# Performance work log

Measured on AMD Instinct MI355X. Metric: run time of the kernel, lower is better.

Reference implementation:

```python
import jax, jax.numpy as jnp
import numpy as np

N = 3        # n_agents (hard-coded by obs.reshape(3,-1) and range(42) loop)
H = 2048     # rnn_hidden_dim
A = 512      # attention_dim
F = 42       # input_shape - n_agents
TAU = 0.01   # gumbel softmax temperature
IDX = np.array([[j for j in range(N) if j != i] for i in range(N)])  # [N, N-1] neighbors in ascending order


def _gru_cell(x, h, Wih, Whh, bih, bhh):
    # PyTorch GRUCell math; weights stacked [r; z; n] along dim 0.
    gi = x @ Wih.T + bih
    gh = h @ Whh.T + bhh
    ir, iz, in_ = jnp.split(gi, 3, axis=-1)
    hr, hz, hn = jnp.split(gh, 3, axis=-1)
    r = jax.nn.sigmoid(ir + hr)
    z = jax.nn.sigmoid(iz + hz)
    n = jnp.tanh(in_ + r * hn)
    return (1.0 - z) * n + z * h


def setup_inputs() -> dict:
    ks = jax.random.split(jax.random.key(0), 24)
    s = 0.02
    rn = lambda k, shp: (jax.random.normal(k, shp) * s).astype(jnp.float32)
    return {
        "obs": jax.random.normal(ks[0], (N, F), dtype=jnp.float32),
        "hidden_state": jax.random.normal(ks[1], (N, H), dtype=jnp.float32),
        "gumbel_noise": jax.random.gumbel(ks[2], (N * (N - 1), 2), dtype=jnp.float32),
        "W_enc": rn(ks[3], (H, F)), "b_enc": rn(ks[4], (H,)),
        "Wih_c": rn(ks[5], (3 * H, H)), "Whh_c": rn(ks[6], (3 * H, H)),
        "bih_c": rn(ks[7], (3 * H,)), "bhh_c": rn(ks[8], (3 * H,)),
        "Wih_f": rn(ks[9], (3 * H, 2 * H)), "Whh_f": rn(ks[10], (3 * H, H)),
        "bih_f": rn(ks[11], (3 * H,)), "bhh_f": rn(ks[12], (3 * H,)),
        "Wih_r": rn(ks[13], (3 * H, 2 * H)), "Whh_r": rn(ks[14], (3 * H, H)),
        "bih_r": rn(ks[15], (3 * H,)), "bhh_r": rn(ks[16], (3 * H,)),
        "W_hard": rn(ks[17], (2, 2 * H)), "b_hard": rn(ks[18], (2,)),
        "Wq": rn(ks[19], (A, H)), "Wk": rn(ks[20], (A, H)),
    }


def reference(obs, hidden_state, gumbel_noise, W_enc, b_enc, Wih_c, Whh_c, bih_c, bhh_c,
              Wih_f, Whh_f, bih_f, bhh_f, Wih_r, Whh_r, bih_r, bhh_r,
              W_hard, b_hard, Wq, Wk):
    # encode + GRUCell step
    x = jax.nn.relu(obs @ W_enc.T + b_enc)                 # [3, H]
    h_out = _gru_cell(x, hidden_state, Wih_c, Whh_c, bih_c, bhh_c)  # [3, H]
    h = h_out.reshape(1, N, H)                              # B=1

    # pairwise concatenations (i, j!=i), seq-major for the bi-GRU
    nbr = h[:, IDX]                                         # [1, N, N-1, H]
    self_rep = jnp.broadcast_to(h[:, :, None, :], nbr.shape)
    pair = jnp.concatenate([self_rep, nbr], axis=-1)        # [1, N, N-1, 2H]
    seq = pair.transpose(2, 0, 1, 3).reshape(N - 1, N, 2 * H)  # [seq=N-1, batch=B*N, 2H]

    h0 = jnp.zeros((N, H), dtype=seq.dtype)

    def step_f(hc, xt):
        hn = _gru_cell(xt, hc, Wih_f, Whh_f, bih_f, bhh_f)
        return hn, hn

    def step_r(hc, xt):
        hn = _gru_cell(xt, hc, Wih_r, Whh_r, bih_r, bhh_r)
        return hn, hn

    _, outs_f = jax.lax.scan(step_f, h0, seq)
    _, outs_r = jax.lax.scan(step_r, h0, seq[::-1])
    h_hard = jnp.concatenate([outs_f, outs_r[::-1]], axis=-1)  # [N-1, N, 2H]
    h_hard = h_hard.transpose(1, 0, 2).reshape(-1, 2 * H)      # [N*(N-1), 2H]

    # hard gate: gumbel-softmax (soft, tau=0.01), take class-1 prob
    logits = h_hard @ W_hard.T + b_hard                      # [N*(N-1), 2]
    y = jax.nn.softmax((logits + gumbel_noise) / TAU, axis=-1)
    hw = y[:, 1].reshape(1, N, 1, N - 1).transpose(1, 0, 2, 3)  # [N, 1, 1, N-1]

    # per-agent masked attention over other agents
    q = (h_out @ Wq.T).reshape(1, N, A)
    k = (h_out @ Wk.T).reshape(1, N, A)
    k_nb = k[:, IDX]                                         # [1, N, N-1, A]
    scores = jnp.einsum('bia,bija->bij', q, k_nb) / jnp.sqrt(jnp.asarray(A, q.dtype))
    soft = jax.nn.softmax(scores, axis=-1)                   # [1, N, N-1]
    xx = soft[0] * hw[:, 0, 0, :]                            # [N, N-1]

    # pairwise squared-distance / duplicate-pair flag logic (vectorized)
    obs3 = obs.reshape(3, -1)                                # [3, 42]
    diff = obs3[:, None, :] - obs3[IDX]                      # [3, 2, 42]
    res = jnp.sum(diff * diff, axis=-1)                      # [3, 2]
    jloc = jnp.argmax(res, axis=1)
    maxv = jnp.take_along_axis(res, jloc[:, None], axis=1)[:, 0]
    iarr = jnp.arange(3)
    jadj = jnp.where((maxv != 0) & (jloc >= iarr), jloc + 1, jloc)
    lo = jnp.minimum(iarr, jadj)
    hi = jnp.maximum(iarr, jadj)
    temp = jnp.stack([lo, hi], axis=-1).astype(jnp.int32)    # [3, 2]
    eq01 = jnp.all(temp[0] == temp[1])
    eq02 = jnp.all(temp[0] == temp[2])
    eq12 = jnp.all(temp[1] == temp[2])
    none = jnp.array([-1, -1], dtype=jnp.int32)              # encodes original flag==0
    flag = jnp.where(eq12, temp[1], jnp.where(eq01 | eq02, temp[0], none))
    return h_out, xx, flag
```

## Files before the change

kernel.cpp:

```cpp
#include <hip/hip_runtime.h>
#include <math.h>

#define HU 2048
#define H3 6144

__device__ __forceinline__ float dot4(float4 a, float4 b){
  return a.x*b.x + a.y*b.y + a.z*b.z + a.w*b.w;
}
__device__ __forceinline__ float wred(float v){
  #pragma unroll
  for (int off = 32; off > 0; off >>= 1) v += __shfl_down(v, off, 64);
  return v;
}
__device__ __forceinline__ float sigm(float x){ return 1.0f/(1.0f + __expf(-x)); }

__global__ void k_enc(const float* __restrict__ obs, const float* __restrict__ W,
                      const float* __restrict__ b, float* __restrict__ x){
  __shared__ float so[128];
  int tid = threadIdx.x;
  if (tid < 126) so[tid] = obs[tid];
  __syncthreads();
  int r = blockIdx.x * blockDim.x + tid;
  if (r < HU){
    const float* wr = W + r*42;
    float a0=0.f, a1=0.f, a2=0.f;
    #pragma unroll
    for (int k2 = 0; k2 < 42; ++k2){
      float w = wr[k2];
      a0 += w*so[k2]; a1 += w*so[42+k2]; a2 += w*so[84+k2];
    }
    float bb = b[r];
    x[r]        = fmaxf(a0+bb, 0.f);
    x[HU + r]   = fmaxf(a1+bb, 0.f);
    x[2*HU + r] = fmaxf(a2+bb, 0.f);
  }
}

__global__ __launch_bounds__(256) void k_gemv2k(
    const float* __restrict__ W0, const float* __restrict__ X0,
    const float* __restrict__ b0, float* __restrict__ O0,
    const float* __restrict__ W1, const float* __restrict__ X1,
    const float* __restrict__ b1, float* __restrict__ O1){
  int blk = blockIdx.x;
  int seg = (blk >= 768);
  const float* W    = seg ? W1 : W0;
  const float* X    = seg ? X1 : X0;
  const float* bias = seg ? b1 : b0;
  float* O          = seg ? O1 : O0;
  int tid = threadIdx.x;
  int wave = tid >> 6, lane = tid & 63;
  int r0 = (((seg ? blk - 768 : blk) * 4 + wave) * 2);
  const float4* W4 = (const float4*)W;
  const float4* X4 = (const float4*)X;
  float acc[2][3];
  acc[0][0]=0.f; acc[0][1]=0.f; acc[0][2]=0.f;
  acc[1][0]=0.f; acc[1][1]=0.f; acc[1][2]=0.f;
  #pragma unroll 2
  for (int win = 0; win < 8; ++win){
    int xi = win*64 + lane;
    float4 x0 = X4[xi], x1 = X4[512 + xi], x2 = X4[1024 + xi];
    float4 w0 = W4[(size_t)r0*512 + xi];
    float4 w1 = W4[(size_t)r0*512 + 512 + xi];
    acc[0][0] += dot4(w0,x0); acc[0][1] += dot4(w0,x1); acc[0][2] += dot4(w0,x2);
    acc[1][0] += dot4(w1,x0); acc[1][1] += dot4(w1,x1); acc[1][2] += dot4(w1,x2);
  }
  #pragma unroll
  for (int j = 0; j < 2; ++j){
    float a0 = wred(acc[j][0]), a1 = wred(acc[j][1]), a2 = wred(acc[j][2]);
    if (lane == 0){
      int row = r0 + j;
      float bb = bias[row];
      O[row] = a0 + bb; O[H3 + row] = a1 + bb; O[2*H3 + row] = a2 + bb;
    }
  }
}

__global__ void k_gate_c(const float* __restrict__ gi, const float* __restrict__ gh,
                         const float* __restrict__ hprev,
                         float* __restrict__ hout_ws, float* __restrict__ dout){
  int id = blockIdx.x * blockDim.x + threadIdx.x;
  if (id >= 3*HU) return;
  int b = id >> 11, u = id & 2047;
  const float* gib = gi + b*H3;
  const float* ghb = gh + b*H3;
  float r = sigm(gib[u]      + ghb[u]);
  float z = sigm(gib[HU+u]   + ghb[HU+u]);
  float n = tanhf(gib[2*HU+u] + r*ghb[2*HU+u]);
  float h = hprev[id];
  float o = (1.f - z)*n + z*h;
  hout_ws[id] = o;
  dout[id] = o;
}

__global__ __launch_bounds__(256) void k_ih(
    const float* __restrict__ Wf, const float* __restrict__ bf, float* __restrict__ giF,
    const float* __restrict__ Wr_, const float* __restrict__ br, float* __restrict__ giR,
    const float* __restrict__ Wq, float* __restrict__ q,
    const float* __restrict__ Wk, float* __restrict__ kk,
    const float* __restrict__ hout){
  int blk = blockIdx.x;
  int tid = threadIdx.x;
  int wave = tid >> 6, lane = tid & 63;
  const float4* X4 = (const float4*)hout;
  if (blk < 1536){
    int segr = (blk >= 768);
    const float* W    = segr ? Wr_ : Wf;
    const float* bias = segr ? br  : bf;
    float* gi         = segr ? giR : giF;
    int r0 = (((segr ? blk - 768 : blk) * 4 + wave) * 2);
    const float4* W4 = (const float4*)W;
    float accS[2][3], accN[2][3];
    accS[0][0]=0.f; accS[0][1]=0.f; accS[0][2]=0.f;
    accS[1][0]=0.f; accS[1][1]=0.f; accS[1][2]=0.f;
    accN[0][0]=0.f; accN[0][1]=0.f; accN[0][2]=0.f;
    accN[1][0]=0.f; accN[1][1]=0.f; accN[1][2]=0.f;
    #pragma unroll 2
    for (int win = 0; win < 8; ++win){
      int xi = win*64 + lane;
      float4 x0 = X4[xi], x1 = X4[512 + xi], x2 = X4[1024 + xi];
      float4 w0 = W4[(size_t)r0*1024 + xi];
      float4 w1 = W4[(size_t)r0*1024 + 1024 + xi];
      accS[0][0] += dot4(w0,x0); accS[0][1] += dot4(w0,x1); accS[0][2] += dot4(w0,x2);
      accS[1][0] += dot4(w1,x0); accS[1][1] += dot4(w1,x1); accS[1][2] += dot4(w1,x2);
    }
    #pragma unroll 2
    for (int win = 0; win < 8; ++win){
      int xi = win*64 + lane;
      float4 x0 = X4[xi], x1 = X4[512 + xi], x2 = X4[1024 + xi];
      float4 w0 = W4[(size_t)r0*1024 + 512 + xi];
      float4 w1 = W4[(size_t)r0*1024 + 1536 + xi];
      accN[0][0] += dot4(w0,x0); accN[0][1] += dot4(w0,x1); accN[0][2] += dot4(w0,x2);
      accN[1][0] += dot4(w1,x0); accN[1][1] += dot4(w1,x1); accN[1][2] += dot4(w1,x2);
    }
    #pragma unroll
    for (int j = 0; j < 2; ++j){
      float s0 = wred(accS[j][0]), s1 = wred(accS[j][1]), s2 = wred(accS[j][2]);
      float n0 = wred(accN[j][0]), n1 = wred(accN[j][1]), n2 = wred(accN[j][2]);
      if (lane == 0){
        int row = r0 + j;
        float bb = bias[row];
        gi[0*H3 + row] = s0 + n1 + bb;
        gi[1*H3 + row] = s1 + n0 + bb;
        gi[2*H3 + row] = s2 + n0 + bb;
        gi[3*H3 + row] = s0 + n2 + bb;
        gi[4*H3 + row] = s1 + n2 + bb;
        gi[5*H3 + row] = s2 + n1 + bb;
      }
    }
  } else {
    int segk = (blk >= 1600);
    const float* W = segk ? Wk : Wq;
    float* O       = segk ? kk : q;
    int r0 = (((segk ? blk - 1600 : blk - 1536) * 4 + wave) * 2);
    const float4* W4 = (const float4*)W;
    float acc[2][3];
    acc[0][0]=0.f; acc[0][1]=0.f; acc[0][2]=0.f;
    acc[1][0]=0.f; acc[1][1]=0.f; acc[1][2]=0.f;
    #pragma unroll 2
    for (int win = 0; win < 8; ++win){
      int xi = win*64 + lane;
      float4 x0 = X4[xi], x1 = X4[512 + xi], x2 = X4[1024 + xi];
      float4 w0 = W4[(size_t)r0*512 + xi];
      float4 w1 = W4[(size_t)r0*512 + 512 + xi];
      acc[0][0] += dot4(w0,x0); acc[0][1] += dot4(w0,x1); acc[0][2] += dot4(w0,x2);
      acc[1][0] += dot4(w1,x0); acc[1][1] += dot4(w1,x1); acc[1][2] += dot4(w1,x2);
    }
    #pragma unroll
    for (int j = 0; j < 2; ++j){
      float a0 = wred(acc[j][0]), a1 = wred(acc[j][1]), a2 = wred(acc[j][2]);
      if (lane == 0){
        int row = r0 + j;
        O[row] = a0; O[512 + row] = a1; O[1024 + row] = a2;
      }
    }
  }
}

__global__ void k_gate0(const float* __restrict__ giF, const float* __restrict__ bhf,
                        float* __restrict__ hf1,
                        const float* __restrict__ giR, const float* __restrict__ bhr,
                        float* __restrict__ hr1){
  int id = blockIdx.x * blockDim.x + threadIdx.x;
  if (id >= 3*HU) return;
  int b = id >> 11, u = id & 2047;
  {
    const float* gib = giF + b*H3;
    float r = sigm(gib[u]      + bhf[u]);
    float z = sigm(gib[HU+u]   + bhf[HU+u]);
    float n = tanhf(gib[2*HU+u] + r*bhf[2*HU+u]);
    hf1[id] = (1.f - z)*n;
  }
  {
    const float* gib = giR + (3 + b)*H3;
    float r = sigm(gib[u]      + bhr[u]);
    float z = sigm(gib[HU+u]   + bhr[HU+u]);
    float n = tanhf(gib[2*HU+u] + r*bhr[2*HU+u]);
    hr1[id] = (1.f - z)*n;
  }
}

__global__ void k_gate1(const float* __restrict__ giF, const float* __restrict__ ghF,
                        const float* __restrict__ hf1, float* __restrict__ hf2,
                        const float* __restrict__ giR, const float* __restrict__ ghR,
                        const float* __restrict__ hr1, float* __restrict__ hr2){
  int id = blockIdx.x * blockDim.x + threadIdx.x;
  if (id >= 3*HU) return;
  int b = id >> 11, u = id & 2047;
  {
    const float* gib = giF + (3 + b)*H3;
    const float* ghb = ghF + b*H3;
    float r = sigm(gib[u]      + ghb[u]);
    float z = sigm(gib[HU+u]   + ghb[HU+u]);
    float n = tanhf(gib[2*HU+u] + r*ghb[2*HU+u]);
    hf2[id] = (1.f - z)*n + z*hf1[id];
  }
  {
    const float* gib = giR + b*H3;
    const float* ghb = ghR + b*H3;
    float r = sigm(gib[u]      + ghb[u]);
    float z = sigm(gib[HU+u]   + ghb[HU+u]);
    float n = tanhf(gib[2*HU+u] + r*ghb[2*HU+u]);
    hr2[id] = (1.f - z)*n + z*hr1[id];
  }
}

__global__ __launch_bounds__(256) void k_final(
    const float* __restrict__ hf1, const float* __restrict__ hf2,
    const float* __restrict__ hr1, const float* __restrict__ hr2,
    const float* __restrict__ q, const float* __restrict__ kk,
    const float* __restrict__ Whard, const float* __restrict__ bhard,
    const float* __restrict__ gumbel, const float* __restrict__ obs,
    float* __restrict__ dout){
  __shared__ float slog[12];
  __shared__ float ssc[6];
  int tid = threadIdx.x;
  int wave = tid >> 6, lane = tid & 63;
  #pragma unroll
  for (int s = 0; s < 3; ++s){
    int d = wave*3 + s;
    int rowi = d >> 1, c = d & 1;
    int i = rowi >> 1, t = rowi & 1;
    const float* F = (t ? hf2 : hf1) + i*HU;
    const float* R = (t ? hr1 : hr2) + i*HU;
    const float* w0 = Whard + c*4096;
    float acc = 0.f;
    for (int j = lane; j < HU; j += 64) acc += w0[j]*F[j] + w0[HU + j]*R[j];
    acc = wred(acc);
    if (lane == 0) slog[d] = acc + bhard[c];
  }
  {
    const int nbr[6] = {1,2, 0,2, 0,1};
    for (int d = wave; d < 6; d += 4){
      int i = d >> 1;
      const float* qv = q + i*512;
      const float* kv = kk + nbr[d]*512;
      float acc = 0.f;
      for (int a = lane; a < 512; a += 64) acc += qv[a]*kv[a];
      acc = wred(acc);
      if (lane == 0) ssc[d] = acc * 0.04419417382415922f;
    }
  }
  __syncthreads();
  if (tid == 0){
    float y1[6];
    #pragma unroll
    for (int rr = 0; rr < 6; ++rr){
      float a0 = (slog[rr*2+0] + gumbel[rr*2+0]) * 100.0f;
      float a1 = (slog[rr*2+1] + gumbel[rr*2+1]) * 100.0f;
      y1[rr] = 1.0f/(1.0f + expf(a0 - a1));
    }
    #pragma unroll
    for (int i = 0; i < 3; ++i){
      float s0 = ssc[i*2], s1 = ssc[i*2+1];
      float m = fmaxf(s0, s1);
      float e0 = expf(s0 - m), e1 = expf(s1 - m);
      float inv = 1.0f/(e0 + e1);
      dout[6144 + i*2 + 0] = e0*inv * y1[i*2 + 0];
      dout[6144 + i*2 + 1] = e1*inv * y1[i*2 + 1];
    }
    const int idx[3][2] = {{1,2},{0,2},{0,1}};
    int temp[3][2];
    #pragma unroll
    for (int i = 0; i < 3; ++i){
      float res[2];
      #pragma unroll
      for (int j = 0; j < 2; ++j){
        float s = 0.f;
        for (int k2 = 0; k2 < 42; ++k2){
          float d2 = obs[i*42 + k2] - obs[idx[i][j]*42 + k2];
          s += d2*d2;
        }
        res[j] = s;
      }
      int jloc = (res[1] > res[0]) ? 1 : 0;
      float maxv = res[jloc];
      int jadj = (maxv != 0.0f && jloc >= i) ? jloc + 1 : jloc;
      int lo = min(i, jadj), hi = max(i, jadj);
      temp[i][0] = lo; temp[i][1] = hi;
    }
    bool eq01 = temp[0][0]==temp[1][0] && temp[0][1]==temp[1][1];
    bool eq02 = temp[0][0]==temp[2][0] && temp[0][1]==temp[2][1];
    bool eq12 = temp[1][0]==temp[2][0] && temp[1][1]==temp[2][1];
    int f0, f1;
    if (eq12){ f0 = temp[1][0]; f1 = temp[1][1]; }
    else if (eq01 || eq02){ f0 = temp[0][0]; f1 = temp[0][1]; }
    else { f0 = -1; f1 = -1; }
    dout[6150] = (float)f0;
    dout[6151] = (float)f1;
  }
}

extern "C" void kernel_launch(void* const* d_in, const int* in_sizes, int n_in,
                              void* d_out, int out_size, void* d_ws, size_t ws_size,
                              hipStream_t stream) {
  const float* obs    = (const float*)d_in[0];
  const float* hidden = (const float*)d_in[1];
  const float* gumbel = (const float*)d_in[2];
  const float* W_enc  = (const float*)d_in[3];
  const float* b_enc  = (const float*)d_in[4];
  const float* Wih_c  = (const float*)d_in[5];
  const float* Whh_c  = (const float*)d_in[6];
  const float* bih_c  = (const float*)d_in[7];
  const float* bhh_c  = (const float*)d_in[8];
  const float* Wih_f  = (const float*)d_in[9];
  const float* Whh_f  = (const float*)d_in[10];
  const float* bih_f  = (const float*)d_in[11];
  const float* bhh_f  = (const float*)d_in[12];
  const float* Wih_r  = (const float*)d_in[13];
  const float* Whh_r  = (const float*)d_in[14];
  const float* bih_r  = (const float*)d_in[15];
  const float* bhh_r  = (const float*)d_in[16];
  const float* W_hard = (const float*)d_in[17];
  const float* b_hard = (const float*)d_in[18];
  const float* Wq     = (const float*)d_in[19];
  const float* Wk     = (const float*)d_in[20];

  float* out = (float*)d_out;
  float* ws  = (float*)d_ws;
  float* x    = ws;
  float* hout = ws + 6144;
  float* gic  = ws + 12288;
  float* ghc  = ws + 30720;
  float* gif  = ws + 49152;
  float* gir  = ws + 86016;
  float* ghf  = ws + 122880;
  float* ghr  = ws + 141312;
  float* hf1  = ws + 159744;
  float* hr1  = ws + 165888;
  float* hf2  = ws + 172032;
  float* hr2  = ws + 178176;
  float* q    = ws + 184320;
  float* kk   = ws + 185856;

  k_enc<<<8, 256, 0, stream>>>(obs, W_enc, b_enc, x);
  k_gemv2k<<<1536, 256, 0, stream>>>(Wih_c, x, bih_c, gic, Whh_c, hidden, bhh_c, ghc);
  k_gate_c<<<24, 256, 0, stream>>>(gic, ghc, hidden, hout, out);
  k_ih<<<1664, 256, 0, stream>>>(Wih_f, bih_f, gif, Wih_r, bih_r, gir, Wq, q, Wk, kk, hout);
  k_gate0<<<24, 256, 0, stream>>>(gif, bhh_f, hf1, gir, bhh_r, hr1);
  k_gemv2k<<<1536, 256, 0, stream>>>(Whh_f, hf1, bhh_f, ghf, Whh_r, hr1, bhh_r, ghr);
  k_gate1<<<24, 256, 0, stream>>>(gif, ghf, hf1, hf2, gir, ghr, hr1, hr2);
  k_final<<<1, 256, 0, stream>>>(hf1, hf2, hr1, hr2, q, kk, W_hard, b_hard, gumbel, obs, out);
}
```

Baseline: 147.9 us.

## Stage GEMV input vector in LDS and double-buffer weights via direct global-to-LDS loads

In the GRU gemv kernels, each block now copies the input vectors into shared memory once. Weight rows are streamed into a per-wave double buffer using `global_load_lds` async copies, with explicit `vmcnt` waits so the next chunk loads while the current one is computed. The aim is to hide global-load latency and avoid repeated X reads from cache. In exchange, each block now uses about 40KB of LDS, which limits occupancy, and only one stage is prefetched ahead. That may mean fewer loads in flight than the previous unrolled register loads.

```diff
diff --git a/kernel.cpp b/kernel.cpp
--- a/kernel.cpp
+++ b/kernel.cpp
@@ -3,6 +3,12 @@
 
 #define HU 2048
 #define H3 6144
+
+typedef const __attribute__((address_space(1))) void* gptr1_t;
+typedef __attribute__((address_space(3))) void* lptr3_t;
+__device__ __forceinline__ void gl_lds16(const void* g, void* l){
+  __builtin_amdgcn_global_load_lds((gptr1_t)g, (lptr3_t)l, 16, 0, 0);
+}
 
 __device__ __forceinline__ float dot4(float4 a, float4 b){
   return a.x*b.x + a.y*b.y + a.z*b.z + a.w*b.w;
@@ -41,26 +47,47 @@
     const float* __restrict__ b0, float* __restrict__ O0,
     const float* __restrict__ W1, const float* __restrict__ X1,
     const float* __restrict__ b1, float* __restrict__ O1){
+  __shared__ float4 shX[1536];
+  __shared__ float4 wbuf[2][512];
   int blk = blockIdx.x;
   int seg = (blk >= 768);
   const float* W    = seg ? W1 : W0;
   const float* X    = seg ? X1 : X0;
   const float* bias = seg ? b1 : b0;
   float* O          = seg ? O1 : O0;
-  int tid = threadIdx.x;
-  int wave = tid >> 6, lane = tid & 63;
-  int r0 = (((seg ? blk - 768 : blk) * 4 + wave) * 2);
-  const float4* W4 = (const float4*)W;
+  int tid = threadIdx.x, wave = tid >> 6, lane = tid & 63;
   const float4* X4 = (const float4*)X;
+  #pragma unroll
+  for (int i = 0; i < 6; ++i) shX[tid + i*256] = X4[tid + i*256];
+  __syncthreads();
+  int rb = (seg ? blk - 768 : blk) * 8;
+  const float* Wr0 = W + (size_t)(rb + wave*2)     * 2048;
+  const float* Wr1 = W + (size_t)(rb + wave*2 + 1) * 2048;
+  float* lds0 = (float*)&wbuf[0][(wave*2+0)*64];
+  float* lds1 = (float*)&wbuf[0][(wave*2+1)*64];
+  float* lds0b = (float*)&wbuf[1][(wave*2+0)*64];
+  float* lds1b = (float*)&wbuf[1][(wave*2+1)*64];
+  gl_lds16(Wr0 + lane*4, lds0);
+  gl_lds16(Wr1 + lane*4, lds1);
   float acc[2][3];
   acc[0][0]=0.f; acc[0][1]=0.f; acc[0][2]=0.f;
   acc[1][0]=0.f; acc[1][1]=0.f; acc[1][2]=0.f;
-  #pragma unroll 2
-  for (int win = 0; win < 8; ++win){
-    int xi = win*64 + lane;
-    float4 x0 = X4[xi], x1 = X4[512 + xi], x2 = X4[1024 + xi];
-    float4 w0 = W4[(size_t)r0*512 + xi];
-    float4 w1 = W4[(size_t)r0*512 + 512 + xi];
+  #pragma unroll
+  for (int s = 0; s < 8; ++s){
+    int b = s & 1;
+    if (s < 7){
+      int off = (s+1)*256 + lane*4;
+      gl_lds16(Wr0 + off, b ? lds0 : lds0b);
+      gl_lds16(Wr1 + off, b ? lds1 : lds1b);
+      asm volatile("s_waitcnt vmcnt(2)" ::: "memory");
+    } else {
+      asm volatile("s_waitcnt vmcnt(0)" ::: "memory");
+    }
+    __builtin_amdgcn_sched_barrier(0);
+    int c = s*64 + lane;
+    float4 x0 = shX[c], x1 = shX[512 + c], x2 = shX[1024 + c];
+    float4 w0 = wbuf[b][(wave*2+0)*64 + lane];
+    float4 w1 = wbuf[b][(wave*2+1)*64 + lane];
     acc[0][0] += dot4(w0,x0); acc[0][1] += dot4(w0,x1); acc[0][2] += dot4(w0,x2);
     acc[1][0] += dot4(w1,x0); acc[1][1] += dot4(w1,x1); acc[1][2] += dot4(w1,x2);
   }
@@ -68,7 +95,7 @@
   for (int j = 0; j < 2; ++j){
     float a0 = wred(acc[j][0]), a1 = wred(acc[j][1]), a2 = wred(acc[j][2]);
     if (lane == 0){
-      int row = r0 + j;
+      int row = rb + wave*2 + j;
       float bb = bias[row];
       O[row] = a0 + bb; O[H3 + row] = a1 + bb; O[2*H3 + row] = a2 + bb;
     }
@@ -98,46 +125,63 @@
     const float* __restrict__ Wq, float* __restrict__ q,
     const float* __restrict__ Wk, float* __restrict__ kk,
     const float* __restrict__ hout){
+  __shared__ float4 shX[1536];
+  __shared__ float4 wbuf[2][512];
   int blk = blockIdx.x;
-  int tid = threadIdx.x;
-  int wave = tid >> 6, lane = tid & 63;
+  int tid = threadIdx.x, wave = tid >> 6, lane = tid & 63;
   const float4* X4 = (const float4*)hout;
+  #pragma unroll
+  for (int i = 0; i < 6; ++i) shX[tid + i*256] = X4[tid + i*256];
+  __syncthreads();
+  float* lds0  = (float*)&wbuf[0][(wave*2+0)*64];
+  float* lds1  = (float*)&wbuf[0][(wave*2+1)*64];
+  float* lds0b = (float*)&wbuf[1][(wave*2+0)*64];
+  float* lds1b = (float*)&wbuf[1][(wave*2+1)*64];
   if (blk < 1536){
     int segr = (blk >= 768);
     const float* W    = segr ? Wr_ : Wf;
     const float* bias = segr ? br  : bf;
     float* gi         = segr ? giR : giF;
-    int r0 = (((segr ? blk - 768 : blk) * 4 + wave) * 2);
-    const float4* W4 = (const float4*)W;
+    int rb = (segr ? blk - 768 : blk) * 8;
+    const float* Wr0 = W + (size_t)(rb + wave*2)     * 4096;
+    const float* Wr1 = W + (size_t)(rb + wave*2 + 1) * 4096;
+    gl_lds16(Wr0 + lane*4, lds0);
+    gl_lds16(Wr1 + lane*4, lds1);
     float accS[2][3], accN[2][3];
     accS[0][0]=0.f; accS[0][1]=0.f; accS[0][2]=0.f;
     accS[1][0]=0.f; accS[1][1]=0.f; accS[1][2]=0.f;
     accN[0][0]=0.f; accN[0][1]=0.f; accN[0][2]=0.f;
     accN[1][0]=0.f; accN[1][1]=0.f; accN[1][2]=0.f;
-    #pragma unroll 2
-    for (int win = 0; win < 8; ++win){
-      int xi = win*64 + lane;
-      float4 x0 = X4[xi], x1 = X4[512 + xi], x2 = X4[1024 + xi];
-      float4 w0 = W4[(size_t)r0*1024 + xi];
-      float4 w1 = W4[(size_t)r0*1024 + 1024 + xi];
-      accS[0][0] += dot4(w0,x0); accS[0][1] += dot4(w0,x1); accS[0][2] += dot4(w0,x2);
-      accS[1][0] += dot4(w1,x0); accS[1][1] += dot4(w1,x1); accS[1][2] += dot4(w1,x2);
-    }
-    #pragma unroll 2
-    for (int win = 0; win < 8; ++win){
-      int xi = win*64 + lane;
-      float4 x0 = X4[xi], x1 = X4[512 + xi], x2 = X4[1024 + xi];
-      float4 w0 = W4[(size_t)r0*1024 + 512 + xi];
-      float4 w1 = W4[(size_t)r0*1024 + 1536 + xi];
-      accN[0][0] += dot4(w0,x0); accN[0][1] += dot4(w0,x1); accN[0][2] += dot4(w0,x2);
-      accN[1][0] += dot4(w1,x0); accN[1][1] += dot4(w1,x1); accN[1][2] += dot4(w1,x2);
+    #pragma unroll
+    for (int s = 0; s < 16; ++s){
+      int b = s & 1;
+      if (s < 15){
+        int off = (s+1)*256 + lane*4;
+        gl_lds16(Wr0 + off, b ? lds0 : lds0b);
+        gl_lds16(Wr1 + off, b ? lds1 : lds1b);
+        asm volatile("s_waitcnt vmcnt(2)" ::: "memory");
+      } else {
+        asm volatile("s_waitcnt vmcnt(0)" ::: "memory");
+      }
+      __builtin_amdgcn_sched_barrier(0);
+      int c = (s & 7)*64 + lane;
+      float4 x0 = shX[c], x1 = shX[512 + c], x2 = shX[1024 + c];
+      float4 w0 = wbuf[b][(wave*2+0)*64 + lane];
+      float4 w1 = wbuf[b][(wave*2+1)*64 + lane];
+      if (s < 8){
+        accS[0][0] += dot4(w0,x0); accS[0][1] += dot4(w0,x1); accS[0][2] += dot4(w0,x2);
+        accS[1][0] += dot4(w1,x0); accS[1][1] += dot4(w1,x1); accS[1][2] += dot4(w1,x2);
+      } else {
+        accN[0][0] += dot4(w0,x0); accN[0][1] += dot4(w0,x1); accN[0][2] += dot4(w0,x2);
+        accN[1][0] += dot4(w1,x0); accN[1][1] += dot4(w1,x1); accN[1][2] += dot4(w1,x2);
+      }
     }
     #pragma unroll
     for (int j = 0; j < 2; ++j){
       float s0 = wred(accS[j][0]), s1 = wred(accS[j][1]), s2 = wred(accS[j][2]);
       float n0 = wred(accN[j][0]), n1 = wred(accN[j][1]), n2 = wred(accN[j][2]);
       if (lane == 0){
-        int row = r0 + j;
+        int row = rb + wave*2 + j;
         float bb = bias[row];
         gi[0*H3 + row] = s0 + n1 + bb;
         gi[1*H3 + row] = s1 + n0 + bb;
@@ -148,20 +192,34 @@
       }
     }
   } else {
-    int segk = (blk >= 1600);
+    int qblk = blk - 1536;
+    int segk = (qblk >= 64);
     const float* W = segk ? Wk : Wq;
     float* O       = segk ? kk : q;
-    int r0 = (((segk ? blk - 1600 : blk - 1536) * 4 + wave) * 2);
-    const float4* W4 = (const float4*)W;
+    int rb = (segk ? qblk - 64 : qblk) * 8;
+    const float* Wr0 = W + (size_t)(rb + wave*2)     * 2048;
+    const float* Wr1 = W + (size_t)(rb + wave*2 + 1) * 2048;
+    gl_lds16(Wr0 + lane*4, lds0);
+    gl_lds16(Wr1 + lane*4, lds1);
     float acc[2][3];
     acc[0][0]=0.f; acc[0][1]=0.f; acc[0][2]=0.f;
     acc[1][0]=0.f; acc[1][1]=0.f; acc[1][2]=0.f;
-    #pragma unroll 2
-    for (int win = 0; win < 8; ++win){
-      int xi = win*64 + lane;
-      float4 x0 = X4[xi], x1 = X4[512 + xi], x2 = X4[1024 + xi];
-      float4 w0 = W4[(size_t)r0*512 + xi];
-      float4 w1 = W4[(size_t)r0*512 + 512 + xi];
+    #pragma unroll
+    for (int s = 0; s < 8; ++s){
+      int b = s & 1;
+      if (s < 7){
+        int off = (s+1)*256 + lane*4;
+        gl_lds16(Wr0 + off, b ? lds0 : lds0b);
+        gl_lds16(Wr1 + off, b ? lds1 : lds1b);
+        asm volatile("s_waitcnt vmcnt(2)" ::: "memory");
+      } else {
+        asm volatile("s_waitcnt vmcnt(0)" ::: "memory");
+      }
+      __builtin_amdgcn_sched_barrier(0);
+      int c = s*64 + lane;
+      float4 x0 = shX[c], x1 = shX[512 + c], x2 = shX[1024 + c];
+      float4 w0 = wbuf[b][(wave*2+0)*64 + lane];
+      float4 w1 = wbuf[b][(wave*2+1)*64 + lane];
       acc[0][0] += dot4(w0,x0); acc[0][1] += dot4(w0,x1); acc[0][2] += dot4(w0,x2);
       acc[1][0] += dot4(w1,x0); acc[1][1] += dot4(w1,x1); acc[1][2] += dot4(w1,x2);
     }
@@ -169,7 +227,7 @@
     for (int j = 0; j < 2; ++j){
       float a0 = wred(acc[j][0]), a1 = wred(acc[j][1]), a2 = wred(acc[j][2]);
       if (lane == 0){
-        int row = r0 + j;
+        int row = rb + wave*2 + j;
         O[row] = a0; O[512 + row] = a1; O[1024 + row] = a2;
       }
     }
```

New measurement: 172.6 us. +16.7%, slower.
